# Kernel optimization log

Measured on AMD Instinct MI355X. Metric: run time of the kernel, lower is better.

## Reference

```python
import jax, jax.numpy as jnp
import numpy as np

N_NODES = 20000
N_EDGES = 320000
EMB = 256
K_DIFF = 3
BN_EPS = 1e-5


def conv1d(x, w, b, stride):
    # x: [N, Cin, L], w: [Cout, Cin, K]
    y = jax.lax.conv_general_dilated(x, w, window_strides=(stride,), padding='VALID',
                                     dimension_numbers=('NCH', 'OIH', 'NCH'))
    return y + b[None, :, None]


def batchnorm_train(x, gamma, beta):
    # training-mode BatchNorm1d over (N, L) per channel, biased variance
    m = jnp.mean(x, axis=(0, 2), keepdims=True)
    v = jnp.var(x, axis=(0, 2), keepdims=True)
    return (x - m) * jax.lax.rsqrt(v + BN_EPS) * gamma[None, :, None] + beta[None, :, None]


def dconv(X, W, b, row, col, norm_out, norm_in, n):
    # Diffusion convolution (pytorch_geometric_temporal DConv), K hops,
    # forward (out-degree) and backward (in-degree) random walks.
    def prop(x, norm):
        msg = norm[:, None] * x[row]                    # [E, F] gather
        return jax.ops.segment_sum(msg, col, num_segments=n)  # scatter-add to targets

    K = W.shape[1]
    Tx_0 = X
    Tx_1 = X
    H = X @ W[0, 0] + X @ W[1, 0]
    if K > 1:
        Tx_1_o = prop(X, norm_out)
        Tx_1_i = prop(X, norm_in)
        H = H + Tx_1_o @ W[0, 1] + Tx_1_i @ W[1, 1]
    for k in range(2, K):
        Tx_2_o = 2.0 * prop(Tx_1_o, norm_out) - Tx_0
        Tx_2_i = 2.0 * prop(Tx_1_i, norm_in) - Tx_0
        H = H + Tx_2_o @ W[0, k] + Tx_2_i @ W[1, k]
        Tx_0, Tx_1_o, Tx_1_i = Tx_1, Tx_2_o, Tx_2_i
    return H + b


def setup_inputs() -> dict:
    key = jax.random.key(0)
    ks = jax.random.split(key, 16)
    d_in = 2 * EMB  # concat([X, H])
    inp = {
        'x': jax.random.normal(ks[0], (N_NODES, 1, 100), dtype=jnp.float32),
        'edge_index': jax.random.randint(ks[1], (2, N_EDGES), 0, N_NODES, dtype=jnp.int32),
        'hidden_state': jax.random.normal(ks[2], (N_NODES, EMB), dtype=jnp.float32),
        'conv1_w': jax.random.normal(ks[3], (32, 1, 10), dtype=jnp.float32) * 0.2,
        'conv1_b': jnp.zeros((32,), jnp.float32),
        'bn1_gamma': jnp.ones((32,), jnp.float32),
        'bn1_beta': jnp.zeros((32,), jnp.float32),
        'conv2_w': jax.random.normal(ks[4], (32, 32, 10), dtype=jnp.float32) * 0.05,
        'conv2_b': jnp.zeros((32,), jnp.float32),
        'bn2_gamma': jnp.ones((32,), jnp.float32),
        'bn2_beta': jnp.zeros((32,), jnp.float32),
        'W_z': jax.random.normal(ks[5], (2, K_DIFF, d_in, EMB), dtype=jnp.float32) * 0.05,
        'b_z': jnp.zeros((EMB,), jnp.float32),
        'W_r': jax.random.normal(ks[6], (2, K_DIFF, d_in, EMB), dtype=jnp.float32) * 0.05,
        'b_r': jnp.zeros((EMB,), jnp.float32),
        'W_h': jax.random.normal(ks[7], (2, K_DIFF, d_in, EMB), dtype=jnp.float32) * 0.05,
        'b_h': jnp.zeros((EMB,), jnp.float32),
    }
    return inp


def reference(x, edge_index, hidden_state, conv1_w, conv1_b, bn1_gamma, bn1_beta,
              conv2_w, conv2_b, bn2_gamma, bn2_beta, W_z, b_z, W_r, b_r, W_h, b_h):
    n = x.shape[0]
    # CNN embedding: conv -> relu -> bn, twice
    h = batchnorm_train(jax.nn.relu(conv1d(x, conv1_w, conv1_b, 3)), bn1_gamma, bn1_beta)
    h = batchnorm_train(jax.nn.relu(conv1d(h, conv2_w, conv2_b, 3)), bn2_gamma, bn2_beta)
    X = h.reshape(n, -1)  # [N, EMB]

    row, col = edge_index[0], edge_index[1]
    ones = jnp.ones((row.shape[0],), X.dtype)
    deg_out = jax.ops.segment_sum(ones, row, num_segments=n)
    deg_in = jax.ops.segment_sum(ones, col, num_segments=n)
    norm_out = (1.0 / deg_out)[row]
    norm_in = (1.0 / deg_in)[col]

    H0 = hidden_state
    XH = jnp.concatenate([X, H0], axis=1)
    Z = jax.nn.sigmoid(dconv(XH, W_z, b_z, row, col, norm_out, norm_in, n))
    R = jax.nn.sigmoid(dconv(XH, W_r, b_r, row, col, norm_out, norm_in, n))
    XRH = jnp.concatenate([X, R * H0], axis=1)
    H_tilde = jnp.tanh(dconv(XRH, W_h, b_h, row, col, norm_out, norm_in, n))
    H = Z * H0 + (1.0 - Z) * H_tilde
    return jax.nn.relu(H)
```

## Files before the change

kernel.cpp:

```cpp
#include <hip/hip_runtime.h>
#include <cstdint>
#include <cstddef>

#define NN 20000
#define NE 320000

typedef float f32x4 __attribute__((ext_vector_type(4)));
typedef short s16x8 __attribute__((ext_vector_type(8)));

struct KB10 { const unsigned short* p[10]; };
struct PPB { const unsigned short* yo0; const unsigned short* yo1;
             const unsigned short* yi0; const unsigned short* yi1;
             unsigned short* po0; unsigned short* po1;
             unsigned short* pi0; unsigned short* pi1; };

__device__ __forceinline__ unsigned short f2bf(float x){
    unsigned u = __float_as_uint(x);
    unsigned r = (u + 0x7fffu + ((u >> 16) & 1u)) >> 16;
    return (unsigned short)r;
}
__device__ __forceinline__ float bf2f(unsigned short s){
    return __uint_as_float(((unsigned)s) << 16);
}

__device__ __forceinline__ void gl16(const void* g, void* l){
    __builtin_amdgcn_global_load_lds((const __attribute__((address_space(1))) unsigned int*)g,
                                     (__attribute__((address_space(3))) unsigned int*)l, 16, 0, 0);
}


__global__ void k_zero(uint32_t* p, int n){
    int i = blockIdx.x*256 + threadIdx.x;
    if(i < n) p[i] = 0u;
}

__global__ void k_degree(const int* __restrict__ ei, int* degout, int* degin){
    int e = blockIdx.x*256 + threadIdx.x;
    if(e < NE){
        atomicAdd(&degout[ei[e]], 1);
        atomicAdd(&degin[ei[NE+e]], 1);
    }
}

__global__ void k_scan(const int* __restrict__ degin, int* __restrict__ coloff,
                       float* __restrict__ invdegin){
    __shared__ int part[1024];
    int t = threadIdx.x;
    int base = t*20;
    int s = 0;
    for(int k=0;k<20;k++){ int i = base+k; if(i < NN) s += degin[i]; }
    part[t] = s;
    __syncthreads();
    for(int off=1; off<1024; off<<=1){
        int v = (t>=off) ? part[t-off] : 0;
        __syncthreads();
        part[t] += v;
        __syncthreads();
    }
    int run = (t>0) ? part[t-1] : 0;
    for(int k=0;k<20;k++){
        int i = base+k;
        if(i < NN){
            int d = degin[i];
            coloff[i] = run;
            run += d;
            invdegin[i] = (d>0) ? (1.0f/(float)d) : 0.0f;
        }
    }
    if(t==1023) coloff[NN] = part[1023];
}

__global__ void k_csr(const int* __restrict__ ei, const int* __restrict__ degout,
                      const int* __restrict__ coloff, int* cnt,
                      int* __restrict__ esrc, float* __restrict__ enormo){
    int e = blockIdx.x*256 + threadIdx.x;
    if(e < NE){
        int r = ei[e], c = ei[NE+e];
        int pos = coloff[c] + atomicAdd(&cnt[c], 1);
        esrc[pos] = r;
        enormo[pos] = 1.0f/(float)degout[r];
    }
}


__global__ void k_conv1(const float* __restrict__ x, const float* __restrict__ w1,
                        const float* __restrict__ b1, unsigned short* __restrict__ y1b){
    __shared__ float w[320];
    __shared__ float bb[32];
    int t = threadIdx.x;
    for(int i=t;i<320;i+=256) w[i] = w1[i];
    if(t < 32) bb[t] = b1[t];
    __syncthreads();
    int gid = blockIdx.x*256 + t;
    if(gid >= NN*31) return;
    int node = gid/31, p = gid - node*31;
    const float* xr = x + node*100 + 3*p;
    float xv[10];
    #pragma unroll
    for(int k=0;k<10;k++) xv[k] = xr[k];
    unsigned short* yo = y1b + (size_t)node*1024 + p;
    #pragma unroll
    for(int c=0;c<32;c++){
        float a = bb[c];
        #pragma unroll
        for(int k=0;k<10;k++) a = fmaf(w[c*10+k], xv[k], a);
        yo[c*32] = f2bf(fmaxf(a, 0.0f));
    }
    if(p == 0){
        #pragma unroll
        for(int c=0;c<32;c++) y1b[(size_t)node*1024 + c*32 + 31] = 0;
    }
}

template<int SLOTS, int PPC>
__global__ void k_chanstats_bf(const unsigned short* __restrict__ y, float* __restrict__ sq){
    int tid = blockIdx.x*blockDim.x + threadIdx.x;
    int slot = tid & (SLOTS-1);
    int node0 = tid / SLOTS;
    int nstride = (gridDim.x*blockDim.x) / SLOTS;
    int c = slot / PPC;
    float s = 0.f, q = 0.f;
    for(int n=node0; n<NN; n+=nstride){
        float v = bf2f(y[(size_t)n*SLOTS + slot]);
        s += v; q = fmaf(v, v, q);
    }
    #pragma unroll
    for(int m=PPC>>1; m>0; m>>=1){
        s += __shfl_xor(s, m);
        q += __shfl_xor(q, m);
    }
    if((threadIdx.x & (PPC-1)) == 0){
        atomicAdd(&sq[c], s);
        atomicAdd(&sq[32+c], q);
    }
}

__global__ void k_bnfin(const float* __restrict__ sq, const float* __restrict__ gamma,
                        const float* __restrict__ beta, float* __restrict__ scsh,
                        float inv_count){
    int c = threadIdx.x;
    if(c < 32){
        float m = sq[c]*inv_count;
        float v = sq[32+c]*inv_count - m*m;
        float sc = gamma[c]*rsqrtf(v + 1e-5f);
        scsh[c] = sc;
        scsh[32+c] = beta[c] - m*sc;
    }
}

__global__ void __launch_bounds__(256) k_conv2(const unsigned short* __restrict__ y1b,
                        const float* __restrict__ w2, const float* __restrict__ b2,
                        const float* __restrict__ scsh1, unsigned short* __restrict__ Xpre){
    __shared__ float wlds[10240];
    __shared__ float hlds[8*1040];
    int t = threadIdx.x;
    int node0 = blockIdx.x*8;
    #pragma unroll
    for(int j=0;j<40;j++){
        int idx = j*256 + t;
        int ck = idx>>5, c2 = idx&31;
        wlds[ck*32 + c2] = w2[c2*320 + ck];
    }
    #pragma unroll
    for(int j=0;j<32;j++){
        int idx = j*256 + t;
        int nl = idx>>10, i = idx&1023;
        int c = i>>5;
        hlds[nl*1040 + i] = fmaf(scsh1[c], bf2f(y1b[(size_t)(node0+nl)*1024 + i]), scsh1[32+c]);
    }
    __syncthreads();
    int nl = t>>5, c2 = t&31;
    int hbase = nl*1040;
    float acc[8];
    float b = b2[c2];
    #pragma unroll
    for(int p=0;p<8;p++) acc[p] = b;
    for(int c=0;c<32;c++){
        float wr[10];
        #pragma unroll
        for(int k=0;k<10;k++) wr[k] = wlds[(c*10+k)*32 + c2];
        float hv[32];
        #pragma unroll
        for(int q=0;q<8;q++){
            float4 v = *(const float4*)&hlds[hbase + c*32 + q*4];
            hv[q*4+0]=v.x; hv[q*4+1]=v.y; hv[q*4+2]=v.z; hv[q*4+3]=v.w;
        }
        #pragma unroll
        for(int p=0;p<8;p++){
            #pragma unroll
            for(int k=0;k<10;k++)
                acc[p] = fmaf(wr[k], hv[3*p+k], acc[p]);
        }
    }
    uint4 pk;
    pk.x = ((unsigned)f2bf(fmaxf(acc[1],0.f))<<16) | f2bf(fmaxf(acc[0],0.f));
    pk.y = ((unsigned)f2bf(fmaxf(acc[3],0.f))<<16) | f2bf(fmaxf(acc[2],0.f));
    pk.z = ((unsigned)f2bf(fmaxf(acc[5],0.f))<<16) | f2bf(fmaxf(acc[4],0.f));
    pk.w = ((unsigned)f2bf(fmaxf(acc[7],0.f))<<16) | f2bf(fmaxf(acc[6],0.f));
    *(uint4*)&Xpre[(size_t)(node0+nl)*256 + c2*8] = pk;
}

__global__ void k_prep(const unsigned short* __restrict__ Xpre, const float* __restrict__ scsh,
                       const float* __restrict__ h0, unsigned short* __restrict__ Xb,
                       unsigned short* __restrict__ h0b){
    int gid = blockIdx.x*256 + threadIdx.x;
    int c = (gid & 255) >> 3;
    Xb[gid] = f2bf(fmaf(scsh[c], bf2f(Xpre[gid]), scsh[32+c]));
    h0b[gid] = f2bf(h0[gid]);
}


__device__ __forceinline__ float weff_val(const float* W, int term, size_t base){
    const size_t S = 512*256;
    if(term==0)      return W[0*S+base] + W[3*S+base] - W[2*S+base] - W[5*S+base];
    else if(term==1) return W[1*S+base];
    else if(term==2) return W[4*S+base];
    else if(term==3) return 2.0f*W[2*S+base];
    else             return 2.0f*W[5*S+base];
}

__global__ void k_weff_zr_t(const float* __restrict__ Wz, const float* __restrict__ Wr,
                            unsigned short* __restrict__ Wt){
    int k = blockIdx.x*256 + threadIdx.x;
    int col = blockIdx.y;
    const float* W = (col < 256) ? Wz : Wr;
    int j = col & 255;
    int kb = k >> 8, rr = k & 255;
    size_t base = (size_t)((kb & 1)*256 + rr)*256 + j;
    Wt[(size_t)col*2560 + k] = f2bf(weff_val(W, kb>>1, base));
}

__global__ void k_weff_h_t(const float* __restrict__ Wh, unsigned short* __restrict__ Wt){
    int k = blockIdx.x*256 + threadIdx.x;
    int col = blockIdx.y;
    int kb = k >> 8, rr = k & 255;
    size_t base = (size_t)((kb & 1)*256 + rr)*256 + col;
    Wt[(size_t)col*2560 + k] = f2bf(weff_val(Wh, kb>>1, base));
}


__device__ __forceinline__ void upd(uint2 u, float w, float* ao4, float* ai4){
    float f0 = __uint_as_float(u.x << 16), f1 = __uint_as_float(u.x & 0xffff0000u);
    float f2 = __uint_as_float(u.y << 16), f3 = __uint_as_float(u.y & 0xffff0000u);
    ao4[0] = fmaf(w, f0, ao4[0]); ao4[1] = fmaf(w, f1, ao4[1]);
    ao4[2] = fmaf(w, f2, ao4[2]); ao4[3] = fmaf(w, f3, ao4[3]);
    ai4[0] += f0; ai4[1] += f1; ai4[2] += f2; ai4[3] += f3;
}
__device__ __forceinline__ void upd2(uint2 uo, uint2 ui, float w, float* ao4, float* ai4){
    float o0 = __uint_as_float(uo.x << 16), o1 = __uint_as_float(uo.x & 0xffff0000u);
    float o2 = __uint_as_float(uo.y << 16), o3 = __uint_as_float(uo.y & 0xffff0000u);
    float i0 = __uint_as_float(ui.x << 16), i1 = __uint_as_float(ui.x & 0xffff0000u);
    float i2 = __uint_as_float(ui.y << 16), i3 = __uint_as_float(ui.y & 0xffff0000u);
    ao4[0] = fmaf(w, o0, ao4[0]); ao4[1] = fmaf(w, o1, ao4[1]);
    ao4[2] = fmaf(w, o2, ao4[2]); ao4[3] = fmaf(w, o3, ao4[3]);
    ai4[0] += i0; ai4[1] += i1; ai4[2] += i2; ai4[3] += i3;
}

template<int NB, bool SAME>
__global__ void __launch_bounds__(256) k_prop(PPB a,
        const int* __restrict__ coloff, const int* __restrict__ esrc,
        const float* __restrict__ enormo, const float* __restrict__ invdegin){
    int node = blockIdx.x*4 + (threadIdx.x>>6);
    if(node >= NN) return;
    int lane = threadIdx.x & 63;
    int s = coloff[node], e = coloff[node+1];
    float ao[NB][4], ai[NB][4];
    #pragma unroll
    for(int b=0;b<NB;b++){
        #pragma unroll
        for(int q=0;q<4;q++){ ao[b][q]=0.f; ai[b][q]=0.f; }
    }
    const unsigned short* yo[2] = {a.yo0, a.yo1};
    const unsigned short* yi[2] = {a.yi0, a.yi1};
    int j = s;
    for(; j+3 < e; j += 4){
        int e0=esrc[j], e1=esrc[j+1], e2=esrc[j+2], e3=esrc[j+3];
        float w0=enormo[j], w1=enormo[j+1], w2=enormo[j+2], w3=enormo[j+3];
        size_t o0=(size_t)e0*256+lane*4, o1=(size_t)e1*256+lane*4;
        size_t o2=(size_t)e2*256+lane*4, o3=(size_t)e3*256+lane*4;
        uint2 A0[NB], A1[NB], A2[NB], A3[NB];
        #pragma unroll
        for(int b=0;b<NB;b++){
            A0[b]=*(const uint2*)(yo[b]+o0); A1[b]=*(const uint2*)(yo[b]+o1);
            A2[b]=*(const uint2*)(yo[b]+o2); A3[b]=*(const uint2*)(yo[b]+o3);
        }
        if(SAME){
            #pragma unroll
            for(int b=0;b<NB;b++){
                upd(A0[b], w0, ao[b], ai[b]); upd(A1[b], w1, ao[b], ai[b]);
                upd(A2[b], w2, ao[b], ai[b]); upd(A3[b], w3, ao[b], ai[b]);
            }
        }else{
            uint2 B0[NB], B1[NB], B2[NB], B3[NB];
            #pragma unroll
            for(int b=0;b<NB;b++){
                B0[b]=*(const uint2*)(yi[b]+o0); B1[b]=*(const uint2*)(yi[b]+o1);
                B2[b]=*(const uint2*)(yi[b]+o2); B3[b]=*(const uint2*)(yi[b]+o3);
            }
            #pragma unroll
            for(int b=0;b<NB;b++){
                upd2(A0[b], B0[b], w0, ao[b], ai[b]); upd2(A1[b], B1[b], w1, ao[b], ai[b]);
                upd2(A2[b], B2[b], w2, ao[b], ai[b]); upd2(A3[b], B3[b], w3, ao[b], ai[b]);
            }
        }
    }
    for(; j < e; j++){
        size_t off = (size_t)esrc[j]*256 + lane*4;
        float w = enormo[j];
        #pragma unroll
        for(int b=0;b<NB;b++){
            uint2 uo = *(const uint2*)(yo[b] + off);
            if(SAME) upd(uo, w, ao[b], ai[b]);
            else{
                uint2 ui = *(const uint2*)(yi[b] + off);
                upd2(uo, ui, w, ao[b], ai[b]);
            }
        }
    }
    float wi = invdegin[node];
    unsigned short* po[2] = {a.po0, a.po1};
    unsigned short* pi[2] = {a.pi0, a.pi1};
    size_t oo = (size_t)node*256 + lane*4;
    #pragma unroll
    for(int b=0;b<NB;b++){
        uint2 o, q;
        o.x = ((unsigned)f2bf(ao[b][1])<<16) | f2bf(ao[b][0]);
        o.y = ((unsigned)f2bf(ao[b][3])<<16) | f2bf(ao[b][2]);
        q.x = ((unsigned)f2bf(wi*ai[b][1])<<16) | f2bf(wi*ai[b][0]);
        q.y = ((unsigned)f2bf(wi*ai[b][3])<<16) | f2bf(wi*ai[b][2]);
        *(uint2*)(po[b] + oo) = o;
        *(uint2*)(pi[b] + oo) = q;
    }
}


template<int MODE, int BNT>
__global__ void __launch_bounds__(256) k_gemm(KB10 blocks, const unsigned short* __restrict__ Wt,
        const float* __restrict__ bias0, const float* __restrict__ bias1,
        const float* __restrict__ h0, const float* __restrict__ Zin,
        float* __restrict__ out0, unsigned short* __restrict__ out1){
    constexpr int WN = BNT/32;
    constexpr int NBCH = BNT*8/256;
    __shared__ unsigned short As[128*64];
    __shared__ unsigned short Bs[BNT*64];
    int t = threadIdx.x;
    int wid = t >> 6, lane = t & 63;
    int l15 = lane & 15, kg = lane >> 4;

    int bid = blockIdx.x;
    int xcd = bid & 7, sblk = bid >> 3;
    int cidx = sblk & 3, r = (sblk >> 2)*8 + xcd;
    if(r >= 157) return;
    int row0 = r*128, col0 = cidx*BNT;
    int rowbase = (wid >> 1)*64, colbase = (wid & 1)*(BNT/2);

    int rcA[4], sgA[4], graA[4];
    #pragma unroll
    for(int i=0;i<4;i++){
        int c = t + i*256;
        rcA[i] = c >> 3;
        sgA[i] = (c & 7) ^ (rcA[i] & 7);
        int gr = row0 + rcA[i];
        graA[i] = (gr < NN) ? gr : NN-1;
    }

    f32x4 acc[4][WN] = {};

    for(int kb=0; kb<10; kb++){
        const unsigned short* Ap = blocks.p[kb];
        const unsigned short* Wp = Wt + (size_t)kb*256;
        for(int kt=0; kt<256; kt+=64){
            #pragma unroll
            for(int i=0;i<4;i++)
                gl16(Ap + (size_t)graA[i]*256 + kt + sgA[i]*8, As + (t+i*256)*8);
            #pragma unroll
            for(int i=0;i<NBCH;i++)
                gl16(Wp + (size_t)(col0+rcA[i])*2560 + kt + sgA[i]*8, Bs + (t+i*256)*8);
            __syncthreads();
            #pragma unroll
            for(int ks=0;ks<2;ks++){
                s16x8 af[4], bfr[WN];
                #pragma unroll
                for(int i=0;i<4;i++){
                    int row = rowbase + i*16 + l15;
                    af[i] = *(const s16x8*)&As[(row*8 + ((ks*4+kg) ^ (row&7)))*8];
                }
                #pragma unroll
                for(int n=0;n<WN;n++){
                    int colr = colbase + n*16 + l15;
                    bfr[n] = *(const s16x8*)&Bs[(colr*8 + ((ks*4+kg) ^ (colr&7)))*8];
                }
                #pragma unroll
                for(int mi=0;mi<4;mi++){
                    #pragma unroll
                    for(int ni=0;ni<WN;ni++){
                        acc[mi][ni] = __builtin_amdgcn_mfma_f32_16x16x32_bf16(
                            af[mi], bfr[ni], acc[mi][ni], 0, 0, 0);
                    }
                }
            }
            __syncthreads();
        }
    }

    #pragma unroll
    for(int mi=0;mi<4;mi++){
        int gr0 = row0 + rowbase + mi*16 + kg*4;
        #pragma unroll
        for(int ni=0;ni<WN;ni++){
            int j = col0 + colbase + ni*16 + l15;
            #pragma unroll
            for(int rr=0;rr<4;rr++){
                int gr = gr0 + rr;
                if(gr < NN){
                    float a = acc[mi][ni][rr];
                    if(MODE == 0){
                        if(j < 256){
                            out0[(size_t)gr*256 + j] = 1.0f/(1.0f + expf(-(a + bias0[j])));
                        }else{
                            int jj = j - 256;
                            float rv = 1.0f/(1.0f + expf(-(a + bias1[jj])));
                            out1[(size_t)gr*256 + jj] = f2bf(rv * h0[(size_t)gr*256 + jj]);
                        }
                    }else{
                        float z = Zin[(size_t)gr*256 + j];
                        float ht = tanhf(a + bias0[j]);
                        float H = z*h0[(size_t)gr*256 + j] + (1.0f - z)*ht;
                        out0[(size_t)gr*256 + j] = fmaxf(H, 0.0f);
                    }
                }
            }
        }
    }
}


extern "C" void kernel_launch(void* const* d_in, const int* in_sizes, int n_in,
                              void* d_out, int out_size, void* d_ws, size_t ws_size,
                              hipStream_t stream){
    const float* x   = (const float*)d_in[0];
    const int*   ei  = (const int*)  d_in[1];
    const float* h0  = (const float*)d_in[2];
    const float* w1  = (const float*)d_in[3];
    const float* b1  = (const float*)d_in[4];
    const float* g1  = (const float*)d_in[5];
    const float* be1 = (const float*)d_in[6];
    const float* w2  = (const float*)d_in[7];
    const float* b2  = (const float*)d_in[8];
    const float* g2  = (const float*)d_in[9];
    const float* be2 = (const float*)d_in[10];
    const float* Wz  = (const float*)d_in[11];
    const float* bz  = (const float*)d_in[12];
    const float* Wr  = (const float*)d_in[13];
    const float* br  = (const float*)d_in[14];
    const float* Wh  = (const float*)d_in[15];
    const float* bh  = (const float*)d_in[16];
    float* out = (float*)d_out;
    float* wsf = (float*)d_ws;
    (void)in_sizes; (void)n_in; (void)out_size;

    const size_t O_DEGO=0, O_DEGI=20000, O_CNT=40000, O_BN=60000;
    const size_t O_COLOFF=60288, O_ESRC=80384, O_ENORMO=400384, O_INVDEG=720384;
    const size_t O_WTZR=740480, O_WTH=1395840;
    const size_t O_XF=1723520;
    const size_t O_XB=6843520, O_H0B=9403520;
    const size_t O_T1OX=11963520, O_T1IX=14523520, O_P2OX=17083520, O_P2IX=19643520;
    const size_t O_HS0=22203520, O_HS1=24763520, O_HS2=27323520, O_HS3=29883520;
    const size_t O_RH=32443520, O_Z=35003520;
    const size_t WS_NEED_BYTES = (size_t)40123520 * 4;
    if(ws_size < WS_NEED_BYTES) return;

    int* degout = (int*)(wsf + O_DEGO);
    int* degin  = (int*)(wsf + O_DEGI);
    int* cnt    = (int*)(wsf + O_CNT);
    float* bn   = wsf + O_BN;
    int* coloff = (int*)(wsf + O_COLOFF);
    int* esrc   = (int*)(wsf + O_ESRC);
    float* enormo = wsf + O_ENORMO;
    float* invdeg = wsf + O_INVDEG;
    unsigned short* Wtzr = (unsigned short*)(wsf + O_WTZR);
    unsigned short* Wth  = (unsigned short*)(wsf + O_WTH);
    unsigned short* Xpre = (unsigned short*)(wsf + O_XF);
    unsigned short* Xb   = (unsigned short*)(wsf + O_XB);
    unsigned short* h0b  = (unsigned short*)(wsf + O_H0B);
    unsigned short* T1oX = (unsigned short*)(wsf + O_T1OX);
    unsigned short* T1iX = (unsigned short*)(wsf + O_T1IX);
    unsigned short* P2oX = (unsigned short*)(wsf + O_P2OX);
    unsigned short* P2iX = (unsigned short*)(wsf + O_P2IX);
    unsigned short* HS0  = (unsigned short*)(wsf + O_HS0);
    unsigned short* HS1  = (unsigned short*)(wsf + O_HS1);
    unsigned short* HS2  = (unsigned short*)(wsf + O_HS2);
    unsigned short* HS3  = (unsigned short*)(wsf + O_HS3);
    unsigned short* RH   = (unsigned short*)(wsf + O_RH);
    float* Z = wsf + O_Z;
    unsigned short* y1b = (unsigned short*)(wsf + O_T1OX);

    k_zero<<<236,256,0,stream>>>((uint32_t*)(wsf + O_DEGO), 60256);
    k_degree<<<1250,256,0,stream>>>(ei, degout, degin);
    k_scan<<<1,1024,0,stream>>>(degin, coloff, invdeg);
    k_csr<<<1250,256,0,stream>>>(ei, degout, coloff, cnt, esrc, enormo);

    k_conv1<<<2422,256,0,stream>>>(x, w1, b1, y1b);
    k_chanstats_bf<1024,32><<<256,256,0,stream>>>(y1b, bn+0);
    k_bnfin<<<1,32,0,stream>>>(bn+0, g1, be1, bn+64, 1.0f/620000.0f);
    k_conv2<<<2500,256,0,stream>>>(y1b, w2, b2, bn+64, Xpre);
    k_chanstats_bf<256,8><<<64,256,0,stream>>>(Xpre, bn+128);
    k_bnfin<<<1,32,0,stream>>>(bn+128, g2, be2, bn+192, 1.0f/160000.0f);
    k_prep<<<20000,256,0,stream>>>(Xpre, bn+192, h0, Xb, h0b);

    k_weff_zr_t<<<dim3(10,512),256,0,stream>>>(Wz, Wr, Wtzr);
    k_weff_h_t<<<dim3(10,256),256,0,stream>>>(Wh, Wth);

    PPB p1; p1.yo0=Xb; p1.yo1=h0b; p1.yi0=Xb; p1.yi1=h0b;
    p1.po0=T1oX; p1.po1=HS0; p1.pi0=T1iX; p1.pi1=HS1;
    k_prop<2,true><<<5000,256,0,stream>>>(p1, coloff, esrc, enormo, invdeg);

    PPB p2; p2.yo0=T1oX; p2.yo1=HS0; p2.yi0=T1iX; p2.yi1=HS1;
    p2.po0=P2oX; p2.po1=HS2; p2.pi0=P2iX; p2.pi1=HS3;
    k_prop<2,false><<<5000,256,0,stream>>>(p2, coloff, esrc, enormo, invdeg);

    KB10 bzr = {{ Xb, h0b, T1oX, HS0, T1iX, HS1, P2oX, HS2, P2iX, HS3 }};
    k_gemm<0,128><<<640,256,0,stream>>>(bzr, Wtzr, bz, br, h0, nullptr, Z, RH);

    PPB q1; q1.yo0=RH; q1.yo1=nullptr; q1.yi0=RH; q1.yi1=nullptr;
    q1.po0=HS0; q1.po1=nullptr; q1.pi0=HS1; q1.pi1=nullptr;
    k_prop<1,true><<<5000,256,0,stream>>>(q1, coloff, esrc, enormo, invdeg);
    PPB q2; q2.yo0=HS0; q2.yo1=nullptr; q2.yi0=HS1; q2.yi1=nullptr;
    q2.po0=HS2; q2.po1=nullptr; q2.pi0=HS3; q2.pi1=nullptr;
    k_prop<1,false><<<5000,256,0,stream>>>(q2, coloff, esrc, enormo, invdeg);

    KB10 bhh = {{ Xb, RH, T1oX, HS0, T1iX, HS1, P2oX, HS2, P2iX, HS3 }};
    k_gemm<1,64><<<640,256,0,stream>>>(bhh, Wth, bh, nullptr, h0, Z, out, nullptr);
}
```

Before: 769.6 us.

## Interleave node feature blocks, pack edge arrays, and double-buffer the GEMM K loop

```diff
diff --git a/kernel.cpp b/kernel.cpp
--- a/kernel.cpp
+++ b/kernel.cpp
@@ -7,25 +7,57 @@
 
 typedef float f32x4 __attribute__((ext_vector_type(4)));
 typedef short s16x8 __attribute__((ext_vector_type(8)));
-
-struct KB10 { const unsigned short* p[10]; };
-struct PPB { const unsigned short* yo0; const unsigned short* yo1;
-             const unsigned short* yi0; const unsigned short* yi1;
-             unsigned short* po0; unsigned short* po1;
-             unsigned short* pi0; unsigned short* pi1; };
-
-__device__ __forceinline__ unsigned short f2bf(float x){
+typedef unsigned short us;
+
+struct KBd { const us* p; int rs; int cs; };
+struct KB10 { KBd b[10]; };
+
+__device__ __forceinline__ us f2bf(float x){
     unsigned u = __float_as_uint(x);
     unsigned r = (u + 0x7fffu + ((u >> 16) & 1u)) >> 16;
-    return (unsigned short)r;
-}
-__device__ __forceinline__ float bf2f(unsigned short s){
+    return (us)r;
+}
+__device__ __forceinline__ float bf2f(us s){
     return __uint_as_float(((unsigned)s) << 16);
 }
 
 __device__ __forceinline__ void gl16(const void* g, void* l){
     __builtin_amdgcn_global_load_lds((const __attribute__((address_space(1))) unsigned int*)g,
                                      (__attribute__((address_space(3))) unsigned int*)l, 16, 0, 0);
+}
+
+__device__ __forceinline__ void upd8(uint4 v, float w, float* ao, float* ai){
+    float f0=__uint_as_float(v.x<<16), f1=__uint_as_float(v.x&0xffff0000u);
+    float f2=__uint_as_float(v.y<<16), f3=__uint_as_float(v.y&0xffff0000u);
+    float f4=__uint_as_float(v.z<<16), f5=__uint_as_float(v.z&0xffff0000u);
+    float f6=__uint_as_float(v.w<<16), f7=__uint_as_float(v.w&0xffff0000u);
+    ao[0]=fmaf(w,f0,ao[0]); ao[1]=fmaf(w,f1,ao[1]); ao[2]=fmaf(w,f2,ao[2]); ao[3]=fmaf(w,f3,ao[3]);
+    ao[4]=fmaf(w,f4,ao[4]); ao[5]=fmaf(w,f5,ao[5]); ao[6]=fmaf(w,f6,ao[6]); ao[7]=fmaf(w,f7,ao[7]);
+    ai[0]+=f0; ai[1]+=f1; ai[2]+=f2; ai[3]+=f3; ai[4]+=f4; ai[5]+=f5; ai[6]+=f6; ai[7]+=f7;
+}
+__device__ __forceinline__ void updw(uint4 v, float w, float* a){
+    float f0=__uint_as_float(v.x<<16), f1=__uint_as_float(v.x&0xffff0000u);
+    float f2=__uint_as_float(v.y<<16), f3=__uint_as_float(v.y&0xffff0000u);
+    float f4=__uint_as_float(v.z<<16), f5=__uint_as_float(v.z&0xffff0000u);
+    float f6=__uint_as_float(v.w<<16), f7=__uint_as_float(v.w&0xffff0000u);
+    a[0]=fmaf(w,f0,a[0]); a[1]=fmaf(w,f1,a[1]); a[2]=fmaf(w,f2,a[2]); a[3]=fmaf(w,f3,a[3]);
+    a[4]=fmaf(w,f4,a[4]); a[5]=fmaf(w,f5,a[5]); a[6]=fmaf(w,f6,a[6]); a[7]=fmaf(w,f7,a[7]);
+}
+__device__ __forceinline__ uint4 pack8(const float* a){
+    uint4 r;
+    r.x=((unsigned)f2bf(a[1])<<16)|f2bf(a[0]);
+    r.y=((unsigned)f2bf(a[3])<<16)|f2bf(a[2]);
+    r.z=((unsigned)f2bf(a[5])<<16)|f2bf(a[4]);
+    r.w=((unsigned)f2bf(a[7])<<16)|f2bf(a[6]);
+    return r;
+}
+__device__ __forceinline__ uint4 pack8s(const float* a, float s){
+    uint4 r;
+    r.x=((unsigned)f2bf(s*a[1])<<16)|f2bf(s*a[0]);
+    r.y=((unsigned)f2bf(s*a[3])<<16)|f2bf(s*a[2]);
+    r.z=((unsigned)f2bf(s*a[5])<<16)|f2bf(s*a[4]);
+    r.w=((unsigned)f2bf(s*a[7])<<16)|f2bf(s*a[6]);
+    return r;
 }
 
 
@@ -71,20 +103,19 @@
 }
 
 __global__ void k_csr(const int* __restrict__ ei, const int* __restrict__ degout,
-                      const int* __restrict__ coloff, int* cnt,
-                      int* __restrict__ esrc, float* __restrict__ enormo){
+                      const int* __restrict__ coloff, int* cnt, int2* __restrict__ ew){
     int e = blockIdx.x*256 + threadIdx.x;
     if(e < NE){
         int r = ei[e], c = ei[NE+e];
         int pos = coloff[c] + atomicAdd(&cnt[c], 1);
-        esrc[pos] = r;
-        enormo[pos] = 1.0f/(float)degout[r];
+        int2 v; v.x = r; v.y = __float_as_int(1.0f/(float)degout[r]);
+        ew[pos] = v;
     }
 }
 
 
 __global__ void k_conv1(const float* __restrict__ x, const float* __restrict__ w1,
-                        const float* __restrict__ b1, unsigned short* __restrict__ y1b){
+                        const float* __restrict__ b1, us* __restrict__ y1b){
     __shared__ float w[320];
     __shared__ float bb[32];
     int t = threadIdx.x;
@@ -98,7 +129,7 @@
     float xv[10];
     #pragma unroll
     for(int k=0;k<10;k++) xv[k] = xr[k];
-    unsigned short* yo = y1b + (size_t)node*1024 + p;
+    us* yo = y1b + (size_t)node*1024 + p;
     #pragma unroll
     for(int c=0;c<32;c++){
         float a = bb[c];
@@ -113,7 +144,7 @@
 }
 
 template<int SLOTS, int PPC>
-__global__ void k_chanstats_bf(const unsigned short* __restrict__ y, float* __restrict__ sq){
+__global__ void k_chanstats_bf(const us* __restrict__ y, float* __restrict__ sq){
     int tid = blockIdx.x*blockDim.x + threadIdx.x;
     int slot = tid & (SLOTS-1);
     int node0 = tid / SLOTS;
@@ -148,9 +179,9 @@
     }
 }
 
-__global__ void __launch_bounds__(256) k_conv2(const unsigned short* __restrict__ y1b,
+__global__ void __launch_bounds__(256) k_conv2(const us* __restrict__ y1b,
                         const float* __restrict__ w2, const float* __restrict__ b2,
-                        const float* __restrict__ scsh1, unsigned short* __restrict__ Xpre){
+                        const float* __restrict__ scsh1, us* __restrict__ Xpre){
     __shared__ float wlds[10240];
     __shared__ float hlds[8*1040];
     int t = threadIdx.x;
@@ -200,13 +231,30 @@
     *(uint4*)&Xpre[(size_t)(node0+nl)*256 + c2*8] = pk;
 }
 
-__global__ void k_prep(const unsigned short* __restrict__ Xpre, const float* __restrict__ scsh,
-                       const float* __restrict__ h0, unsigned short* __restrict__ Xb,
-                       unsigned short* __restrict__ h0b){
-    int gid = blockIdx.x*256 + threadIdx.x;
-    int c = (gid & 255) >> 3;
-    Xb[gid] = f2bf(fmaf(scsh[c], bf2f(Xpre[gid]), scsh[32+c]));
-    h0b[gid] = f2bf(h0[gid]);
+__global__ void __launch_bounds__(256) k_prep(const us* __restrict__ Xpre,
+        const float* __restrict__ scsh, const float* __restrict__ h0,
+        us* __restrict__ XHp){
+    int node = blockIdx.x*4 + (threadIdx.x>>6);
+    if(node >= NN) return;
+    int lane = threadIdx.x & 63;
+    int half = lane>>5, g = lane&31;
+    uint4 o;
+    if(half == 0){
+        uint4 v = *(const uint4*)(Xpre + (size_t)node*256 + g*8);
+        float sc = scsh[g], sh = scsh[32+g];
+        float y[8];
+        y[0]=fmaf(sc,__uint_as_float(v.x<<16),sh); y[1]=fmaf(sc,__uint_as_float(v.x&0xffff0000u),sh);
+        y[2]=fmaf(sc,__uint_as_float(v.y<<16),sh); y[3]=fmaf(sc,__uint_as_float(v.y&0xffff0000u),sh);
+        y[4]=fmaf(sc,__uint_as_float(v.z<<16),sh); y[5]=fmaf(sc,__uint_as_float(v.z&0xffff0000u),sh);
+        y[6]=fmaf(sc,__uint_as_float(v.w<<16),sh); y[7]=fmaf(sc,__uint_as_float(v.w&0xffff0000u),sh);
+        o = pack8(y);
+    }else{
+        float4 a = *(const float4*)(h0 + (size_t)node*256 + g*8);
+        float4 b = *(const float4*)(h0 + (size_t)node*256 + g*8 + 4);
+        float y[8] = {a.x,a.y,a.z,a.w,b.x,b.y,b.z,b.w};
+        o = pack8(y);
+    }
+    *(uint4*)(XHp + (size_t)node*512 + (size_t)g*16 + half*8) = o;
 }
 
 
@@ -220,7 +268,7 @@
 }
 
 __global__ void k_weff_zr_t(const float* __restrict__ Wz, const float* __restrict__ Wr,
-                            unsigned short* __restrict__ Wt){
+                            us* __restrict__ Wt){
     int k = blockIdx.x*256 + threadIdx.x;
     int col = blockIdx.y;
     const float* W = (col < 256) ? Wz : Wr;
@@ -230,7 +278,7 @@
     Wt[(size_t)col*2560 + k] = f2bf(weff_val(W, kb>>1, base));
 }
 
-__global__ void k_weff_h_t(const float* __restrict__ Wh, unsigned short* __restrict__ Wt){
+__global__ void k_weff_h_t(const float* __restrict__ Wh, us* __restrict__ Wt){
     int k = blockIdx.x*256 + threadIdx.x;
     int col = blockIdx.y;
     int kb = k >> 8, rr = k & 255;
@@ -239,110 +287,141 @@
 }
 
 
-__device__ __forceinline__ void upd(uint2 u, float w, float* ao4, float* ai4){
-    float f0 = __uint_as_float(u.x << 16), f1 = __uint_as_float(u.x & 0xffff0000u);
-    float f2 = __uint_as_float(u.y << 16), f3 = __uint_as_float(u.y & 0xffff0000u);
-    ao4[0] = fmaf(w, f0, ao4[0]); ao4[1] = fmaf(w, f1, ao4[1]);
-    ao4[2] = fmaf(w, f2, ao4[2]); ao4[3] = fmaf(w, f3, ao4[3]);
-    ai4[0] += f0; ai4[1] += f1; ai4[2] += f2; ai4[3] += f3;
-}
-__device__ __forceinline__ void upd2(uint2 uo, uint2 ui, float w, float* ao4, float* ai4){
-    float o0 = __uint_as_float(uo.x << 16), o1 = __uint_as_float(uo.x & 0xffff0000u);
-    float o2 = __uint_as_float(uo.y << 16), o3 = __uint_as_float(uo.y & 0xffff0000u);
-    float i0 = __uint_as_float(ui.x << 16), i1 = __uint_as_float(ui.x & 0xffff0000u);
-    float i2 = __uint_as_float(ui.y << 16), i3 = __uint_as_float(ui.y & 0xffff0000u);
-    ao4[0] = fmaf(w, o0, ao4[0]); ao4[1] = fmaf(w, o1, ao4[1]);
-    ao4[2] = fmaf(w, o2, ao4[2]); ao4[3] = fmaf(w, o3, ao4[3]);
-    ai4[0] += i0; ai4[1] += i1; ai4[2] += i2; ai4[3] += i3;
-}
-
-template<int NB, bool SAME>
-__global__ void __launch_bounds__(256) k_prop(PPB a,
-        const int* __restrict__ coloff, const int* __restrict__ esrc,
-        const float* __restrict__ enormo, const float* __restrict__ invdegin){
+__global__ void __launch_bounds__(256) k_prop1(const us* __restrict__ XHp,
+        const int* __restrict__ coloff, const int2* __restrict__ ew,
+        const float* __restrict__ invdeg, us* __restrict__ T1op, us* __restrict__ T1ip){
     int node = blockIdx.x*4 + (threadIdx.x>>6);
     if(node >= NN) return;
     int lane = threadIdx.x & 63;
+    size_t lo = (size_t)(lane&31)*16 + (lane>>5)*8;
     int s = coloff[node], e = coloff[node+1];
-    float ao[NB][4], ai[NB][4];
-    #pragma unroll
-    for(int b=0;b<NB;b++){
-        #pragma unroll
-        for(int q=0;q<4;q++){ ao[b][q]=0.f; ai[b][q]=0.f; }
-    }
-    const unsigned short* yo[2] = {a.yo0, a.yo1};
-    const unsigned short* yi[2] = {a.yi0, a.yi1};
+    float ao[8]={0,0,0,0,0,0,0,0}, ai[8]={0,0,0,0,0,0,0,0};
     int j = s;
     for(; j+3 < e; j += 4){
-        int e0=esrc[j], e1=esrc[j+1], e2=esrc[j+2], e3=esrc[j+3];
-        float w0=enormo[j], w1=enormo[j+1], w2=enormo[j+2], w3=enormo[j+3];
-        size_t o0=(size_t)e0*256+lane*4, o1=(size_t)e1*256+lane*4;
-        size_t o2=(size_t)e2*256+lane*4, o3=(size_t)e3*256+lane*4;
-        uint2 A0[NB], A1[NB], A2[NB], A3[NB];
-        #pragma unroll
-        for(int b=0;b<NB;b++){
-            A0[b]=*(const uint2*)(yo[b]+o0); A1[b]=*(const uint2*)(yo[b]+o1);
-            A2[b]=*(const uint2*)(yo[b]+o2); A3[b]=*(const uint2*)(yo[b]+o3);
-        }
-        if(SAME){
-            #pragma unroll
-            for(int b=0;b<NB;b++){
-                upd(A0[b], w0, ao[b], ai[b]); upd(A1[b], w1, ao[b], ai[b]);
-                upd(A2[b], w2, ao[b], ai[b]); upd(A3[b], w3, ao[b], ai[b]);
-            }
-        }else{
-            uint2 B0[NB], B1[NB], B2[NB], B3[NB];
-            #pragma unroll
-            for(int b=0;b<NB;b++){
-                B0[b]=*(const uint2*)(yi[b]+o0); B1[b]=*(const uint2*)(yi[b]+o1);
-                B2[b]=*(const uint2*)(yi[b]+o2); B3[b]=*(const uint2*)(yi[b]+o3);
-            }
-            #pragma unroll
-            for(int b=0;b<NB;b++){
-                upd2(A0[b], B0[b], w0, ao[b], ai[b]); upd2(A1[b], B1[b], w1, ao[b], ai[b]);
-                upd2(A2[b], B2[b], w2, ao[b], ai[b]); upd2(A3[b], B3[b], w3, ao[b], ai[b]);
-            }
-        }
+        int2 e0=ew[j], e1=ew[j+1], e2=ew[j+2], e3=ew[j+3];
+        uint4 v0=*(const uint4*)(XHp+(size_t)e0.x*512+lo);
+        uint4 v1=*(const uint4*)(XHp+(size_t)e1.x*512+lo);
+        uint4 v2=*(const uint4*)(XHp+(size_t)e2.x*512+lo);
+        uint4 v3=*(const uint4*)(XHp+(size_t)e3.x*512+lo);
+        upd8(v0,__int_as_float(e0.y),ao,ai);
+        upd8(v1,__int_as_float(e1.y),ao,ai);
+        upd8(v2,__int_as_float(e2.y),ao,ai);
+        upd8(v3,__int_as_float(e3.y),ao,ai);
     }
     for(; j < e; j++){
-        size_t off = (size_t)esrc[j]*256 + lane*4;
-        float w = enormo[j];
-        #pragma unroll
-        for(int b=0;b<NB;b++){
-            uint2 uo = *(const uint2*)(yo[b] + off);
-            if(SAME) upd(uo, w, ao[b], ai[b]);
-            else{
-                uint2 ui = *(const uint2*)(yi[b] + off);
-                upd2(uo, ui, w, ao[b], ai[b]);
-            }
-        }
-    }
-    float wi = invdegin[node];
-    unsigned short* po[2] = {a.po0, a.po1};
-    unsigned short* pi[2] = {a.pi0, a.pi1};
-    size_t oo = (size_t)node*256 + lane*4;
-    #pragma unroll
-    for(int b=0;b<NB;b++){
-        uint2 o, q;
-        o.x = ((unsigned)f2bf(ao[b][1])<<16) | f2bf(ao[b][0]);
-        o.y = ((unsigned)f2bf(ao[b][3])<<16) | f2bf(ao[b][2]);
-        q.x = ((unsigned)f2bf(wi*ai[b][1])<<16) | f2bf(wi*ai[b][0]);
-        q.y = ((unsigned)f2bf(wi*ai[b][3])<<16) | f2bf(wi*ai[b][2]);
-        *(uint2*)(po[b] + oo) = o;
-        *(uint2*)(pi[b] + oo) = q;
-    }
+        int2 ed = ew[j];
+        uint4 v = *(const uint4*)(XHp+(size_t)ed.x*512+lo);
+        upd8(v,__int_as_float(ed.y),ao,ai);
+    }
+    float wi = invdeg[node];
+    *(uint4*)(T1op+(size_t)node*512+lo) = pack8(ao);
+    *(uint4*)(T1ip+(size_t)node*512+lo) = pack8s(ai,wi);
+}
+
+__global__ void __launch_bounds__(256) k_prop2(const us* __restrict__ T1op,
+        const us* __restrict__ T1ip,
+        const int* __restrict__ coloff, const int2* __restrict__ ew,
+        const float* __restrict__ invdeg, us* __restrict__ P2op, us* __restrict__ P2ip){
+    int node = blockIdx.x*4 + (threadIdx.x>>6);
+    if(node >= NN) return;
+    int lane = threadIdx.x & 63;
+    size_t lo = (size_t)(lane&31)*16 + (lane>>5)*8;
+    int s = coloff[node], e = coloff[node+1];
+    float ao[8]={0,0,0,0,0,0,0,0}, ai[8]={0,0,0,0,0,0,0,0};
+    int j = s;
+    for(; j+1 < e; j += 2){
+        int2 e0=ew[j], e1=ew[j+1];
+        size_t o0=(size_t)e0.x*512+lo, o1=(size_t)e1.x*512+lo;
+        uint4 a0=*(const uint4*)(T1op+o0), b0=*(const uint4*)(T1ip+o0);
+        uint4 a1=*(const uint4*)(T1op+o1), b1=*(const uint4*)(T1ip+o1);
+        float one = 1.0f;
+        updw(a0,__int_as_float(e0.y),ao); updw(b0,one,ai);
+        updw(a1,__int_as_float(e1.y),ao); updw(b1,one,ai);
+    }
+    if(j < e){
+        int2 ed = ew[j];
+        size_t o0=(size_t)ed.x*512+lo;
+        uint4 a0=*(const uint4*)(T1op+o0), b0=*(const uint4*)(T1ip+o0);
+        updw(a0,__int_as_float(ed.y),ao); updw(b0,1.0f,ai);
+    }
+    float wi = invdeg[node];
+    *(uint4*)(P2op+(size_t)node*512+lo) = pack8(ao);
+    *(uint4*)(P2ip+(size_t)node*512+lo) = pack8s(ai,wi);
+}
+
+__global__ void __launch_bounds__(256) k_propq1(const us* __restrict__ RHb,
+        const int* __restrict__ coloff, const int2* __restrict__ ew,
+        const float* __restrict__ invdeg, us* __restrict__ Q1p){
+    int node = blockIdx.x*4 + (threadIdx.x>>6);
+    if(node >= NN) return;
+    int lane = threadIdx.x & 63;
+    int half = lane>>5, g = lane&31;
+    int s = coloff[node], e = coloff[node+1];
+    float ao[8]={0,0,0,0,0,0,0,0}, ai[8]={0,0,0,0,0,0,0,0};
+    int j = s;
+    for(; j+1 < e; j += 2){
+        int2 ed = ew[j+half];
+        uint4 v = *(const uint4*)(RHb+(size_t)ed.x*256+g*8);
+        upd8(v,__int_as_float(ed.y),ao,ai);
+    }
+    if(j < e && half == 0){
+        int2 ed = ew[j];
+        uint4 v = *(const uint4*)(RHb+(size_t)ed.x*256+g*8);
+        upd8(v,__int_as_float(ed.y),ao,ai);
+    }
+    #pragma unroll
+    for(int k=0;k<8;k++){
+        ao[k] += __shfl_xor(ao[k],32);
+        ai[k] += __shfl_xor(ai[k],32);
+    }
+    if(half == 0){
+        float wi = invdeg[node];
+        *(uint4*)(Q1p+(size_t)node*512+(size_t)g*16)   = pack8(ao);
+        *(uint4*)(Q1p+(size_t)node*512+(size_t)g*16+8) = pack8s(ai,wi);
+    }
+}
+
+__global__ void __launch_bounds__(256) k_propq2(const us* __restrict__ Q1p,
+        const int* __restrict__ coloff, const int2* __restrict__ ew,
+        const float* __restrict__ invdeg, us* __restrict__ Q2p){
+    int node = blockIdx.x*4 + (threadIdx.x>>6);
+    if(node >= NN) return;
+    int lane = threadIdx.x & 63;
+    int half = lane>>5;
+    size_t lo = (size_t)(lane&31)*16 + half*8;
+    int s = coloff[node], e = coloff[node+1];
+    float a[8]={0,0,0,0,0,0,0,0};
+    int j = s;
+    for(; j+3 < e; j += 4){
+        int2 e0=ew[j], e1=ew[j+1], e2=ew[j+2], e3=ew[j+3];
+        uint4 v0=*(const uint4*)(Q1p+(size_t)e0.x*512+lo);
+        uint4 v1=*(const uint4*)(Q1p+(size_t)e1.x*512+lo);
+        uint4 v2=*(const uint4*)(Q1p+(size_t)e2.x*512+lo);
+        uint4 v3=*(const uint4*)(Q1p+(size_t)e3.x*512+lo);
+        updw(v0, half ? 1.0f : __int_as_float(e0.y), a);
+        updw(v1, half ? 1.0f : __int_as_float(e1.y), a);
+        updw(v2, half ? 1.0f : __int_as_float(e2.y), a);
+        updw(v3, half ? 1.0f : __int_as_float(e3.y), a);
+    }
+    for(; j < e; j++){
+        int2 ed = ew[j];
+        uint4 v = *(const uint4*)(Q1p+(size_t)ed.x*512+lo);
+        updw(v, half ? 1.0f : __int_as_float(ed.y), a);
+    }
+    float sc = half ? invdeg[node] : 1.0f;
+    *(uint4*)(Q2p+(size_t)node*512+lo) = pack8s(a,sc);
 }
 
 
 template<int MODE, int BNT>
-__global__ void __launch_bounds__(256) k_gemm(KB10 blocks, const unsigned short* __restrict__ Wt,
+__global__ void __launch_bounds__(256) k_gemm(KB10 blocks, const us* __restrict__ Wt,
         const float* __restrict__ bias0, const float* __restrict__ bias1,
         const float* __restrict__ h0, const float* __restrict__ Zin,
-        float* __restrict__ out0, unsigned short* __restrict__ out1){
+        float* __restrict__ out0, us* __restrict__ out1){
     constexpr int WN = BNT/32;
-    constexpr int NBCH = BNT*8/256;
-    __shared__ unsigned short As[128*64];
-    __shared__ unsigned short Bs[BNT*64];
+    constexpr int NB = BNT/64;
+    __shared__ us As[2][4096];
+    __shared__ us Bs[2][BNT*32];
     int t = threadIdx.x;
     int wid = t >> 6, lane = t & 63;
     int l15 = lane & 15, kg = lane >> 4;
@@ -353,54 +432,66 @@
     if(r >= 157) return;
     int row0 = r*128, col0 = cidx*BNT;
     int rowbase = (wid >> 1)*64, colbase = (wid & 1)*(BNT/2);
-
-    int rcA[4], sgA[4], graA[4];
-    #pragma unroll
-    for(int i=0;i<4;i++){
+    int swz = (l15 >> 1) & 3;
+
+    int srA[2], sgA[2], graA[2];
+    #pragma unroll
+    for(int i=0;i<2;i++){
         int c = t + i*256;
-        rcA[i] = c >> 3;
-        sgA[i] = (c & 7) ^ (rcA[i] & 7);
-        int gr = row0 + rcA[i];
+        srA[i] = c >> 2;
+        sgA[i] = (c & 3) ^ ((srA[i] >> 1) & 3);
+        int gr = row0 + srA[i];
         graA[i] = (gr < NN) ? gr : NN-1;
     }
+    int srB[NB], sgB[NB];
+    #pragma unroll
+    for(int i=0;i<NB;i++){
+        int c = t + i*256;
+        srB[i] = c >> 2;
+        sgB[i] = (c & 3) ^ ((srB[i] >> 1) & 3);
+    }
 
     f32x4 acc[4][WN] = {};
 
-    for(int kb=0; kb<10; kb++){
-        const unsigned short* Ap = blocks.p[kb];
-        const unsigned short* Wp = Wt + (size_t)kb*256;
-        for(int kt=0; kt<256; kt+=64){
+    auto stage = [&](int buf, int step){
+        int kb = step >> 3, kt = (step & 7)*32, ktc = (step & 7)*4;
+        const us* Ap = blocks.b[kb].p;
+        int rs = blocks.b[kb].rs, cs = blocks.b[kb].cs;
+        #pragma unroll
+        for(int i=0;i<2;i++)
+            gl16(Ap + (size_t)graA[i]*rs + (size_t)(ktc + sgA[i])*cs, &As[buf][(t+i*256)*8]);
+        const us* Wp = Wt + (size_t)kb*256;
+        #pragma unroll
+        for(int i=0;i<NB;i++)
+            gl16(Wp + (size_t)(col0+srB[i])*2560 + kt + sgB[i]*8, &Bs[buf][(t+i*256)*8]);
+    };
+
+    stage(0, 0);
+    __syncthreads();
+    int cur = 0;
+    for(int step=0; step<80; step++){
+        if(step < 79) stage(cur^1, step+1);
+        s16x8 af[4], bfr[WN];
+        #pragma unroll
+        for(int i=0;i<4;i++){
+            int row = rowbase + i*16 + l15;
+            af[i] = *(const s16x8*)&As[cur][(row*4 + (kg ^ swz))*8];
+        }
+        #pragma unroll
+        for(int n=0;n<WN;n++){
+            int colr = colbase + n*16 + l15;
+            bfr[n] = *(const s16x8*)&Bs[cur][(colr*4 + (kg ^ swz))*8];
+        }
+        #pragma unroll
+        for(int mi=0;mi<4;mi++){
             #pragma unroll
-            for(int i=0;i<4;i++)
-                gl16(Ap + (size_t)graA[i]*256 + kt + sgA[i]*8, As + (t+i*256)*8);
-            #pragma unroll
-            for(int i=0;i<NBCH;i++)
-                gl16(Wp + (size_t)(col0+rcA[i])*2560 + kt + sgA[i]*8, Bs + (t+i*256)*8);
-            __syncthreads();
-            #pragma unroll
-            for(int ks=0;ks<2;ks++){
-                s16x8 af[4], bfr[WN];
-                #pragma unroll
-                for(int i=0;i<4;i++){
-                    int row = rowbase + i*16 + l15;
-                    af[i] = *(const s16x8*)&As[(row*8 + ((ks*4+kg) ^ (row&7)))*8];
-                }
-                #pragma unroll
-                for(int n=0;n<WN;n++){
-                    int colr = colbase + n*16 + l15;
-                    bfr[n] = *(const s16x8*)&Bs[(colr*8 + ((ks*4+kg) ^ (colr&7)))*8];
-                }
-                #pragma unroll
-                for(int mi=0;mi<4;mi++){
-                    #pragma unroll
-                    for(int ni=0;ni<WN;ni++){
-                        acc[mi][ni] = __builtin_amdgcn_mfma_f32_16x16x32_bf16(
-                            af[mi], bfr[ni], acc[mi][ni], 0, 0, 0);
-                    }
-                }
+            for(int ni=0;ni<WN;ni++){
+                acc[mi][ni] = __builtin_amdgcn_mfma_f32_16x16x32_bf16(
+                    af[mi], bfr[ni], acc[mi][ni], 0, 0, 0);
             }
-            __syncthreads();
         }
+        __syncthreads();
+        cur ^= 1;
     }
 
     #pragma unroll
@@ -460,14 +551,14 @@
     (void)in_sizes; (void)n_in; (void)out_size;
 
     const size_t O_DEGO=0, O_DEGI=20000, O_CNT=40000, O_BN=60000;
-    const size_t O_COLOFF=60288, O_ESRC=80384, O_ENORMO=400384, O_INVDEG=720384;
+    const size_t O_COLOFF=60288, O_EW=80384, O_INVDEG=720384;
     const size_t O_WTZR=740480, O_WTH=1395840;
-    const size_t O_XF=1723520;
-    const size_t O_XB=6843520, O_H0B=9403520;
-    const size_t O_T1OX=11963520, O_T1IX=14523520, O_P2OX=17083520, O_P2IX=19643520;
-    const size_t O_HS0=22203520, O_HS1=24763520, O_HS2=27323520, O_HS3=29883520;
-    const size_t O_RH=32443520, O_Z=35003520;
-    const size_t WS_NEED_BYTES = (size_t)40123520 * 4;
+    const size_t O_XPRE=1723520;
+    const size_t O_XHP=4283520;
+    const size_t O_T1OP=9403520, O_T1IP=14523520, O_P2OP=19643520, O_P2IP=24763520;
+    const size_t O_Q1P=29883520, O_Q2P=35003520;
+    const size_t O_RH=40123520, O_Z=42683520;
+    const size_t WS_NEED_BYTES = (size_t)47803520 * 4;
     if(ws_size < WS_NEED_BYTES) return;
 
     int* degout = (int*)(wsf + O_DEGO);
@@ -475,30 +566,26 @@
     int* cnt    = (int*)(wsf + O_CNT);
     float* bn   = wsf + O_BN;
     int* coloff = (int*)(wsf + O_COLOFF);
-    int* esrc   = (int*)(wsf + O_ESRC);
-    float* enormo = wsf + O_ENORMO;
+    int2* ew    = (int2*)(wsf + O_EW);
     float* invdeg = wsf + O_INVDEG;
-    unsigned short* Wtzr = (unsigned short*)(wsf + O_WTZR);
-    unsigned short* Wth  = (unsigned short*)(wsf + O_WTH);
-    unsigned short* Xpre = (unsigned short*)(wsf + O_XF);
-    unsigned short* Xb   = (unsigned short*)(wsf + O_XB);
-    unsigned short* h0b  = (unsigned short*)(wsf + O_H0B);
-    unsigned short* T1oX = (unsigned short*)(wsf + O_T1OX);
-    unsigned short* T1iX = (unsigned short*)(wsf + O_T1IX);
-    unsigned short* P2oX = (unsigned short*)(wsf + O_P2OX);
-    unsigned short* P2iX = (unsigned short*)(wsf + O_P2IX);
-    unsigned short* HS0  = (unsigned short*)(wsf + O_HS0);
-    unsigned short* HS1  = (unsigned short*)(wsf + O_HS1);
-    unsigned short* HS2  = (unsigned short*)(wsf + O_HS2);
-    unsigned short* HS3  = (unsigned short*)(wsf + O_HS3);
-    unsigned short* RH   = (unsigned short*)(wsf + O_RH);
+    us* Wtzr = (us*)(wsf + O_WTZR);
+    us* Wth  = (us*)(wsf + O_WTH);
+    us* Xpre = (us*)(wsf + O_XPRE);
+    us* XHp  = (us*)(wsf + O_XHP);
+    us* T1op = (us*)(wsf + O_T1OP);
+    us* T1ip = (us*)(wsf + O_T1IP);
+    us* P2op = (us*)(wsf + O_P2OP);
+    us* P2ip = (us*)(wsf + O_P2IP);
+    us* Q1p  = (us*)(wsf + O_Q1P);
+    us* Q2p  = (us*)(wsf + O_Q2P);
+    us* RHb  = (us*)(wsf + O_RH);
     float* Z = wsf + O_Z;
-    unsigned short* y1b = (unsigned short*)(wsf + O_T1OX);
+    us* y1b  = (us*)(wsf + O_T1OP);
 
     k_zero<<<236,256,0,stream>>>((uint32_t*)(wsf + O_DEGO), 60256);
     k_degree<<<1250,256,0,stream>>>(ei, degout, degin);
     k_scan<<<1,1024,0,stream>>>(degin, coloff, invdeg);
-    k_csr<<<1250,256,0,stream>>>(ei, degout, coloff, cnt, esrc, enormo);
+    k_csr<<<1250,256,0,stream>>>(ei, degout, coloff, cnt, ew);
 
     k_conv1<<<2422,256,0,stream>>>(x, w1, b1, y1b);
     k_chanstats_bf<1024,32><<<256,256,0,stream>>>(y1b, bn+0);
@@ -506,29 +593,24 @@
     k_conv2<<<2500,256,0,stream>>>(y1b, w2, b2, bn+64, Xpre);
     k_chanstats_bf<256,8><<<64,256,0,stream>>>(Xpre, bn+128);
     k_bnfin<<<1,32,0,stream>>>(bn+128, g2, be2, bn+192, 1.0f/160000.0f);
-    k_prep<<<20000,256,0,stream>>>(Xpre, bn+192, h0, Xb, h0b);
+    k_prep<<<5000,256,0,stream>>>(Xpre, bn+192, h0, XHp);
 
     k_weff_zr_t<<<dim3(10,512),256,0,stream>>>(Wz, Wr, Wtzr);
     k_weff_h_t<<<dim3(10,256),256,0,stream>>>(Wh, Wth);
 
-    PPB p1; p1.yo0=Xb; p1.yo1=h0b; p1.yi0=Xb; p1.yi1=h0b;
-    p1.po0=T1oX; p1.po1=HS0; p1.pi0=T1iX; p1.pi1=HS1;
-    k_prop<2,true><<<5000,256,0,stream>>>(p1, coloff, esrc, enormo, invdeg);
-
-    PPB p2; p2.yo0=T1oX; p2.yo1=HS0; p2.yi0=T1iX; p2.yi1=HS1;
-    p2.po0=P2oX; p2.po1=HS2; p2.pi0=P2iX; p2.pi1=HS3;
-    k_prop<2,false><<<5000,256,0,stream>>>(p2, coloff, esrc, enormo, invdeg);
-
-    KB10 bzr = {{ Xb, h0b, T1oX, HS0, T1iX, HS1, P2oX, HS2, P2iX, HS3 }};
-    k_gemm<0,128><<<640,256,0,stream>>>(bzr, Wtzr, bz, br, h0, nullptr, Z, RH);
-
-    PPB q1; q1.yo0=RH; q1.yo1=nullptr; q1.yi0=RH; q1.yi1=nullptr;
-    q1.po0=HS0; q1.po1=nullptr; q1.pi0=HS1; q1.pi1=nullptr;
-    k_prop<1,true><<<5000,256,0,stream>>>(q1, coloff, esrc, enormo, invdeg);
-    PPB q2; q2.yo0=HS0; q2.yo1=nullptr; q2.yi0=HS1; q2.yi1=nullptr;
-    q2.po0=HS2; q2.po1=nullptr; q2.pi0=HS3; q2.pi1=nullptr;
-    k_prop<1,false><<<5000,256,0,stream>>>(q2, coloff, esrc, enormo, invdeg);
-
-    KB10 bhh = {{ Xb, RH, T1oX, HS0, T1iX, HS1, P2oX, HS2, P2iX, HS3 }};
+    k_prop1<<<5000,256,0,stream>>>(XHp, coloff, ew, invdeg, T1op, T1ip);
+    k_prop2<<<5000,256,0,stream>>>(T1op, T1ip, coloff, ew, invdeg, P2op, P2ip);
+
+    KB10 bzr = {{ {XHp,512,16},{XHp+8,512,16},{T1op,512,16},{T1op+8,512,16},
+                  {T1ip,512,16},{T1ip+8,512,16},{P2op,512,16},{P2op+8,512,16},
+                  {P2ip,512,16},{P2ip+8,512,16} }};
+    k_gemm<0,128><<<640,256,0,stream>>>(bzr, Wtzr, bz, br, h0, nullptr, Z, RHb);
+
+    k_propq1<<<5000,256,0,stream>>>(RHb, coloff, ew, invdeg, Q1p);
+    k_propq2<<<5000,256,0,stream>>>(Q1p, coloff, ew, invdeg, Q2p);
+
+    KB10 bhh = {{ {XHp,512,16},{RHb,256,8},{T1op,512,16},{Q1p,512,16},
+                  {T1ip,512,16},{Q1p+8,512,16},{P2op,512,16},{Q2p,512,16},
+                  {P2ip,512,16},{Q2p+8,512,16} }};
     k_gemm<1,64><<<640,256,0,stream>>>(bhh, Wth, bh, nullptr, h0, Z, out, nullptr);
 }
```

New measurement: 791.7 us. 1.03x slower.
